# Kernel tuning notes

Hardware: AMD Instinct MI355X
Metric: run time of the kernel (lower is better)

The kernel has to match this reference:

```python
import jax, jax.numpy as jnp
import numpy as np


def setup_inputs() -> dict:
    key = jax.random.key(0)
    k_x, k_rbf, k_nb, k_w1, k_w2 = jax.random.split(key, 5)
    N, NB, F_DIM, RBF_DIM = 20000, 32, 128, 64
    x = jax.random.normal(k_x, (N, F_DIM), dtype=jnp.float32)
    rbf = jax.random.uniform(k_rbf, (N, NB, RBF_DIM), dtype=jnp.float32)
    neighbors = jax.random.randint(k_nb, (N, NB), 0, N, dtype=jnp.int64)
    # filter network params (Linear(rbf_dim->f_dim), Softplus, Linear(f_dim->f_dim))
    w1 = jax.random.normal(k_w1, (RBF_DIM, F_DIM), dtype=jnp.float32) / np.sqrt(RBF_DIM)
    b1 = jnp.zeros((F_DIM,), dtype=jnp.float32)
    w2 = jax.random.normal(k_w2, (F_DIM, F_DIM), dtype=jnp.float32) / np.sqrt(F_DIM)
    b2 = jnp.zeros((F_DIM,), dtype=jnp.float32)
    return {"x": x, "rbf": rbf, "neighbors": neighbors,
            "w1": w1, "b1": b1, "w2": w2, "b2": b2}


def reference(x, rbf, neighbors, w1, b1, w2, b2):
    # filter network: Linear -> Softplus -> Linear, applied per (atom, neighbor)
    h = jax.nn.softplus(jnp.einsum('anr,rf->anf', rbf, w1) + b1)  # [N, NB, F]
    W = jnp.einsum('ang,gf->anf', h, w2) + b2                      # [N, NB, F]
    x_j = x[neighbors]                                             # gather [N, NB, F]
    return jnp.sum(x_j * W, axis=1)                                # [N, F]
```

## Files before the change

kernel.cpp:

```cpp
#include <hip/hip_runtime.h>
#include <hip/hip_bf16.h>
#include <math.h>


#define NB     32
#define FD     128
#define RD     64
#define WAVES  8
#define NTILES 2500

typedef short  short8  __attribute__((ext_vector_type(8)));
typedef float  floatx4 __attribute__((ext_vector_type(4)));
typedef float  floatx2 __attribute__((ext_vector_type(2)));

#define LDS_FENCE() asm volatile("" ::: "memory")

static __device__ __forceinline__ unsigned pk2(float a, float b) {
  __hip_bfloat162 h = __float22bfloat162_rn(float2{a, b});
  unsigned u;
  __builtin_memcpy(&u, &h, sizeof(u));
  return u;
}

static __device__ __forceinline__ float softplus(float v) {
  return fmaxf(v, 0.0f) + __logf(1.0f + __expf(-fabsf(v)));
}

__global__ __launch_bounds__(512, 4)
void cfconv_kernel(const float* __restrict__ x,
                   const float* __restrict__ rbf,
                   const int*   __restrict__ nbr,
                   const float* __restrict__ w1,
                   const float* __restrict__ b1,
                   const float* __restrict__ w2,
                   const float* __restrict__ b2,
                   float* __restrict__ out) {
  __shared__ __align__(16) short w1f[16][64][8];
  __shared__ __align__(16) short w2f[32][64][8];
  __shared__ __align__(16) short hbuf[WAVES * 16][128];

  const int tid  = threadIdx.x;
  const int lane = tid & 63;
  const int wv   = tid >> 6;
  const int q    = lane >> 4;
  const int ln   = lane & 15;

  for (int i = tid; i < RD * FD; i += 512) {
    int k = i >> 7, n = i & 127, kk = k & 31;
    w1f[(k >> 5) * 8 + (n >> 4)][(kk >> 3) * 16 + (n & 15)][kk & 7] = (short)pk2(w1[i], 0.f);
  }
  for (int i = tid; i < FD * FD; i += 512) {
    int k = i >> 7, n = i & 127, kk = k & 31;
    w2f[(k >> 5) * 8 + (n >> 4)][(kk >> 3) * 16 + (n & 15)][kk & 7] = (short)pk2(w2[i], 0.f);
  }
  float b1v[8], b2v[8];
#pragma unroll
  for (int nt = 0; nt < 8; ++nt) {
    b1v[nt] = b1[nt * 16 + ln];
    b2v[nt] = b2[nt * 16 + ln];
  }
  __syncthreads();

  short (*band)[128] = &hbuf[wv * 16];
  const int cb2 = (lane * 2) >> 3;
  const int cl2 = (lane * 2) & 7;

  for (int tile = blockIdx.x; tile < NTILES; tile += gridDim.x) {
    const int atom = tile * WAVES + wv;
    const int prow = atom * NB;
    const int* nbp = nbr + prow;

    float o0 = 0.f, o1 = 0.f;

#pragma unroll
    for (int mt = 0; mt < 2; ++mt) {
      const float* src = rbf + (prow + mt * 16 + ln) * RD + q * 8;
      short8 afrag[2];
#pragma unroll
      for (int kt = 0; kt < 2; ++kt) {
        floatx4 lo = __builtin_nontemporal_load((const floatx4*)(src + kt * 32));
        floatx4 hi = __builtin_nontemporal_load((const floatx4*)(src + kt * 32 + 4));
        union { short8 s8; unsigned u[4]; } f;
        f.u[0] = pk2(lo[0], lo[1]);
        f.u[1] = pk2(lo[2], lo[3]);
        f.u[2] = pk2(hi[0], hi[1]);
        f.u[3] = pk2(hi[2], hi[3]);
        afrag[kt] = f.s8;
      }

      floatx4 acc[8];
#pragma unroll
      for (int nt = 0; nt < 8; ++nt) acc[nt] = floatx4{0.f, 0.f, 0.f, 0.f};
#pragma unroll
      for (int kt = 0; kt < 2; ++kt)
#pragma unroll
        for (int nt = 0; nt < 8; ++nt) {
          short8 bfrag = *(const short8*)&w1f[kt * 8 + nt][lane][0];
          acc[nt] = __builtin_amdgcn_mfma_f32_16x16x32_bf16(
              afrag[kt], bfrag, acc[nt], 0, 0, 0);
        }

#pragma unroll
      for (int nt = 0; nt < 8; ++nt) {
        const int c  = nt * 16 + ln;
        const int cb = c >> 3, cl = c & 7;
        unsigned u01 = pk2(softplus(acc[nt][0] + b1v[nt]), softplus(acc[nt][1] + b1v[nt]));
        unsigned u23 = pk2(softplus(acc[nt][2] + b1v[nt]), softplus(acc[nt][3] + b1v[nt]));
        band[q * 4 + 0][(((cb ^ (q * 4 + 0)) & 15) << 3) | cl] = (short)u01;
        band[q * 4 + 1][(((cb ^ (q * 4 + 1)) & 15) << 3) | cl] = (short)(u01 >> 16);
        band[q * 4 + 2][(((cb ^ (q * 4 + 2)) & 15) << 3) | cl] = (short)u23;
        band[q * 4 + 3][(((cb ^ (q * 4 + 3)) & 15) << 3) | cl] = (short)(u23 >> 16);
      }
      LDS_FENCE();

      short8 hfrag[4];
#pragma unroll
      for (int kt = 0; kt < 4; ++kt) {
        const int pb = ((kt * 4 + q) ^ ln) & 15;
        hfrag[kt] = *(const short8*)&band[ln][pb << 3];
      }
      LDS_FENCE();

#pragma unroll
      for (int nt = 0; nt < 8; ++nt) acc[nt] = floatx4{0.f, 0.f, 0.f, 0.f};
#pragma unroll
      for (int kt = 0; kt < 4; ++kt)
#pragma unroll
        for (int nt = 0; nt < 8; ++nt) {
          short8 bfrag = *(const short8*)&w2f[kt * 8 + nt][lane][0];
          acc[nt] = __builtin_amdgcn_mfma_f32_16x16x32_bf16(
              hfrag[kt], bfrag, acc[nt], 0, 0, 0);
        }

#pragma unroll
      for (int nt = 0; nt < 8; ++nt) {
        const int c  = nt * 16 + ln;
        const int cb = c >> 3, cl = c & 7;
        unsigned u01 = pk2(acc[nt][0] + b2v[nt], acc[nt][1] + b2v[nt]);
        unsigned u23 = pk2(acc[nt][2] + b2v[nt], acc[nt][3] + b2v[nt]);
        band[q * 4 + 0][(((cb ^ (q * 4 + 0)) & 15) << 3) | cl] = (short)u01;
        band[q * 4 + 1][(((cb ^ (q * 4 + 1)) & 15) << 3) | cl] = (short)(u01 >> 16);
        band[q * 4 + 2][(((cb ^ (q * 4 + 2)) & 15) << 3) | cl] = (short)u23;
        band[q * 4 + 3][(((cb ^ (q * 4 + 3)) & 15) << 3) | cl] = (short)(u23 >> 16);
      }
      LDS_FENCE();

#pragma unroll 4
      for (int r = 0; r < 16; ++r) {
        const int j = nbp[mt * 16 + r];
        floatx2 xv = *(const floatx2*)(x + j * FD + lane * 2);
        unsigned pw;
        __builtin_memcpy(&pw, &band[r][(((cb2 ^ r) & 15) << 3) | cl2], 4);
        o0 = fmaf(xv[0], __builtin_bit_cast(float, pw << 16), o0);
        o1 = fmaf(xv[1], __builtin_bit_cast(float, pw & 0xFFFF0000u), o1);
      }
      LDS_FENCE();
    }

    __builtin_nontemporal_store(floatx2{o0, o1}, (floatx2*)(out + atom * FD + lane * 2));
  }
}

extern "C" void kernel_launch(void* const* d_in, const int* in_sizes, int n_in,
                              void* d_out, int out_size, void* d_ws, size_t ws_size,
                              hipStream_t stream) {
  const float* x   = (const float*)d_in[0];
  const float* rbf = (const float*)d_in[1];
  const int*   nbr = (const int*)d_in[2];
  const float* w1  = (const float*)d_in[3];
  const float* b1  = (const float*)d_in[4];
  const float* w2  = (const float*)d_in[5];
  const float* b2  = (const float*)d_in[6];
  float* out = (float*)d_out;

  cfconv_kernel<<<dim3(500), dim3(512), 0, stream>>>(x, rbf, nbr, w1, b1, w2, b2, out);
}
```

Baseline: 305.6 us.

## Fold log2 scaling into weights for cheaper softplus and prefetch neighbor gathers

Pre-scales w1/b1 by log2(e) and w2 by ln2 so softplus becomes log2(1+exp2(z)) using raw hardware exp2/log intrinsics, removing the max/abs and extra multiplies. It also moves the neighbor x gathers ahead of the two MFMA stages into 16 register pairs, so global-load latency overlaps the matrix work. The direct formula can overflow or lose precision for large positive inputs, and the 32 extra live registers per mt iteration may strain the 512x4 launch bounds.

```diff
diff --git a/kernel.cpp b/kernel.cpp
--- a/kernel.cpp
+++ b/kernel.cpp
@@ -8,6 +8,9 @@
 #define RD     64
 #define WAVES  8
 #define NTILES 2500
+
+#define LOG2E 1.4426950408889634f
+#define LN2   0.6931471805599453f
 
 typedef short  short8  __attribute__((ext_vector_type(8)));
 typedef float  floatx4 __attribute__((ext_vector_type(4)));
@@ -22,8 +25,8 @@
   return u;
 }
 
-static __device__ __forceinline__ float softplus(float v) {
-  return fmaxf(v, 0.0f) + __logf(1.0f + __expf(-fabsf(v)));
+static __device__ __forceinline__ float sp2(float acc) {
+  return __builtin_amdgcn_logf(1.0f + __builtin_amdgcn_exp2f(acc));
 }
 
 __global__ __launch_bounds__(512, 4)
@@ -47,16 +50,18 @@
 
   for (int i = tid; i < RD * FD; i += 512) {
     int k = i >> 7, n = i & 127, kk = k & 31;
-    w1f[(k >> 5) * 8 + (n >> 4)][(kk >> 3) * 16 + (n & 15)][kk & 7] = (short)pk2(w1[i], 0.f);
+    w1f[(k >> 5) * 8 + (n >> 4)][(kk >> 3) * 16 + (n & 15)][kk & 7] =
+        (short)pk2(w1[i] * LOG2E, 0.f);
   }
   for (int i = tid; i < FD * FD; i += 512) {
     int k = i >> 7, n = i & 127, kk = k & 31;
-    w2f[(k >> 5) * 8 + (n >> 4)][(kk >> 3) * 16 + (n & 15)][kk & 7] = (short)pk2(w2[i], 0.f);
+    w2f[(k >> 5) * 8 + (n >> 4)][(kk >> 3) * 16 + (n & 15)][kk & 7] =
+        (short)pk2(w2[i] * LN2, 0.f);
   }
   float b1v[8], b2v[8];
 #pragma unroll
   for (int nt = 0; nt < 8; ++nt) {
-    b1v[nt] = b1[nt * 16 + ln];
+    b1v[nt] = b1[nt * 16 + ln] * LOG2E;
     b2v[nt] = b2[nt * 16 + ln];
   }
   __syncthreads();
@@ -88,6 +93,13 @@
         afrag[kt] = f.s8;
       }
 
+      floatx2 xpre[16];
+#pragma unroll
+      for (int r = 0; r < 16; ++r) {
+        const int j = nbp[mt * 16 + r];
+        xpre[r] = *(const floatx2*)(x + j * FD + lane * 2);
+      }
+
       floatx4 acc[8];
 #pragma unroll
       for (int nt = 0; nt < 8; ++nt) acc[nt] = floatx4{0.f, 0.f, 0.f, 0.f};
@@ -104,8 +116,8 @@
       for (int nt = 0; nt < 8; ++nt) {
         const int c  = nt * 16 + ln;
         const int cb = c >> 3, cl = c & 7;
-        unsigned u01 = pk2(softplus(acc[nt][0] + b1v[nt]), softplus(acc[nt][1] + b1v[nt]));
-        unsigned u23 = pk2(softplus(acc[nt][2] + b1v[nt]), softplus(acc[nt][3] + b1v[nt]));
+        unsigned u01 = pk2(sp2(acc[nt][0] + b1v[nt]), sp2(acc[nt][1] + b1v[nt]));
+        unsigned u23 = pk2(sp2(acc[nt][2] + b1v[nt]), sp2(acc[nt][3] + b1v[nt]));
         band[q * 4 + 0][(((cb ^ (q * 4 + 0)) & 15) << 3) | cl] = (short)u01;
         band[q * 4 + 1][(((cb ^ (q * 4 + 1)) & 15) << 3) | cl] = (short)(u01 >> 16);
         band[q * 4 + 2][(((cb ^ (q * 4 + 2)) & 15) << 3) | cl] = (short)u23;
@@ -145,14 +157,12 @@
       }
       LDS_FENCE();
 
-#pragma unroll 4
+#pragma unroll
       for (int r = 0; r < 16; ++r) {
-        const int j = nbp[mt * 16 + r];
-        floatx2 xv = *(const floatx2*)(x + j * FD + lane * 2);
         unsigned pw;
         __builtin_memcpy(&pw, &band[r][(((cb2 ^ r) & 15) << 3) | cl2], 4);
-        o0 = fmaf(xv[0], __builtin_bit_cast(float, pw << 16), o0);
-        o1 = fmaf(xv[1], __builtin_bit_cast(float, pw & 0xFFFF0000u), o1);
+        o0 = fmaf(xpre[r][0], __builtin_bit_cast(float, pw << 16), o0);
+        o1 = fmaf(xpre[r][1], __builtin_bit_cast(float, pw & 0xFFFF0000u), o1);
       }
       LDS_FENCE();
     }
```

After: 418.9 us. +37.1%, slower.
